# Kernel optimization log

Hardware: AMD Instinct MI355X
Metric: run time of the kernel (lower is better)

Reference implementation:

```python
import jax, jax.numpy as jnp
import numpy as np

D_MODEL = 512
N_HEADS = 8
HEAD_DIM = D_MODEL // N_HEADS
SCALE = float(np.sqrt(HEAD_DIM))


def setup_inputs() -> dict:
    key = jax.random.key(0)
    k1, k2, k3, k4, k5, k6 = jax.random.split(key, 6)
    B, T, S = 4, 2048, 4096
    query = jax.random.normal(k1, (B, T, D_MODEL), dtype=jnp.float32)
    keys = jax.random.normal(k2, (B, S, D_MODEL), dtype=jnp.float32)
    key_padding_mask = jnp.zeros((B, S), dtype=bool)  # all valid
    # Linear params (torch nn.Linear: y = x @ W.T + b)
    lim = 1.0 / np.sqrt(D_MODEL)
    q_w = jax.random.uniform(k3, (D_MODEL, D_MODEL), jnp.float32, -lim, lim)
    q_b = jax.random.uniform(k4, (D_MODEL,), jnp.float32, -lim, lim)
    k_w = jax.random.uniform(k5, (D_MODEL, D_MODEL), jnp.float32, -lim, lim)
    k_b = jax.random.uniform(k6, (D_MODEL,), jnp.float32, -lim, lim)
    return {"query": query, "keys": keys, "key_padding_mask": key_padding_mask,
            "q_w": q_w, "q_b": q_b, "k_w": k_w, "k_b": k_b}


def reference(query, keys, key_padding_mask, q_w, q_b, k_w, k_b):
    B, T, _ = query.shape
    S = keys.shape[1]
    q = (query @ q_w.T + q_b).reshape(B, T, N_HEADS, HEAD_DIM)
    k = (keys @ k_w.T + k_b).reshape(B, S, N_HEADS, HEAD_DIM)
    # mean over heads of scaled per-head QK^T == single contraction over (h,d)
    # divided by n_heads*scale; avoids materializing [B,H,T,S].
    logits = jnp.einsum('bthd,bshd->bts', q, k) / (N_HEADS * SCALE)
    logits = jnp.where(key_padding_mask[:, None, :], -jnp.inf, logits)
    return logits
```

## Files before the change

kernel.cpp:

```cpp
#include <hip/hip_runtime.h>
#include <hip/hip_bf16.h>

using bf16 = __hip_bfloat16;
typedef __attribute__((ext_vector_type(8))) short short8;
typedef __attribute__((ext_vector_type(4))) float floatx4;
typedef __attribute__((ext_vector_type(16))) float floatx16;

#define NEG_INF (-__builtin_huge_valf())

__device__ __forceinline__ void gld_lds16(const void* g, void* l) {
  __builtin_amdgcn_global_load_lds(
      (const __attribute__((address_space(1))) unsigned int*)g,
      (__attribute__((address_space(3))) unsigned int*)l, 16, 0, 0);
}

template <int N> __device__ __forceinline__ void wait_vm() {
  asm volatile("s_waitcnt vmcnt(%0)" ::"n"(N) : "memory");
}
__device__ __forceinline__ void bar() {
  asm volatile("" ::: "memory");
  __builtin_amdgcn_s_barrier();
  asm volatile("" ::: "memory");
}

__device__ __forceinline__ void cvt8(const float4& a, const float4& b, bf16* t) {
  t[0] = __float2bfloat16(a.x); t[1] = __float2bfloat16(a.y);
  t[2] = __float2bfloat16(a.z); t[3] = __float2bfloat16(a.w);
  t[4] = __float2bfloat16(b.x); t[5] = __float2bfloat16(b.y);
  t[6] = __float2bfloat16(b.z); t[7] = __float2bfloat16(b.w);
}

__global__ __launch_bounds__(256) void cvt_in(const float* __restrict__ q,
                                              const float* __restrict__ k,
                                              const float* __restrict__ qw,
                                              const float* __restrict__ kw,
                                              bf16* __restrict__ qo, bf16* __restrict__ ko,
                                              bf16* __restrict__ qwo, bf16* __restrict__ kwo) {
  const size_t e = ((size_t)blockIdx.x * 256 + threadIdx.x) * 8;
  const float* src; bf16* dst;
  if (e < 4194304)       { src = q  + e;              dst = qo  + e; }
  else if (e < 12582912) { src = k  + (e - 4194304);  dst = ko  + (e - 4194304); }
  else if (e < 12845056) { src = qw + (e - 12582912); dst = qwo + (e - 12582912); }
  else                   { src = kw + (e - 12845056); dst = kwo + (e - 12845056); }
  float4 a = *(const float4*)src;
  float4 c = *(const float4*)(src + 4);
  bf16 t[8];
  cvt8(a, c, t);
  *(short8*)dst = *(short8*)t;
}

__device__ __forceinline__ void mfma_tile32(const bf16* sAh, const bf16* sBh,
                                            int wm, int wn, int lane,
                                            floatx16 acc[2][2]) {
  const int fm = lane & 31;
  const int fk = (lane >> 5) * 8;
  #pragma unroll
  for (int ks = 0; ks < 2; ++ks) {
    short8 a0 = *(const short8*)(sAh + (wm +  0 + fm) * 32 + ks * 16 + fk);
    short8 a1 = *(const short8*)(sAh + (wm + 32 + fm) * 32 + ks * 16 + fk);
    short8 b0 = *(const short8*)(sBh + (wn +  0 + fm) * 32 + ks * 16 + fk);
    short8 b1 = *(const short8*)(sBh + (wn + 32 + fm) * 32 + ks * 16 + fk);
    acc[0][0] = __builtin_amdgcn_mfma_f32_32x32x16_bf16(a0, b0, acc[0][0], 0, 0, 0);
    acc[0][1] = __builtin_amdgcn_mfma_f32_32x32x16_bf16(a0, b1, acc[0][1], 0, 0, 0);
    acc[1][0] = __builtin_amdgcn_mfma_f32_32x32x16_bf16(a1, b0, acc[1][0], 0, 0, 0);
    acc[1][1] = __builtin_amdgcn_mfma_f32_32x32x16_bf16(a1, b1, acc[1][1], 0, 0, 0);
  }
}

__global__ __launch_bounds__(256) void proj(const bf16* __restrict__ Xq,
                                            const bf16* __restrict__ Xk,
                                            const bf16* __restrict__ qw,
                                            const bf16* __restrict__ kw,
                                            const float* __restrict__ qb,
                                            const float* __restrict__ kb,
                                            bf16* __restrict__ qo,
                                            bf16* __restrict__ ko) {
  __shared__ bf16 sA[2][128 * 32];
  __shared__ bf16 sB[2][128 * 32];
  const int mt = blockIdx.x;
  const bool isQ = mt < 64;
  const bf16* A    = isQ ? Xq : Xk;
  const bf16* W    = isQ ? qw : kw;
  const float* bias = isQ ? qb : kb;
  bf16* outp       = isQ ? qo : ko;
  const int m0 = (isQ ? mt : mt - 64) * 128;
  const int n0 = blockIdx.y * 128;

  const int tid  = threadIdx.x;
  const int lane = tid & 63;
  const int w    = tid >> 6;
  const int wm   = (w >> 1) * 64;
  const int wn   = (w & 1) * 64;
  const int st_row = lane >> 2;
  const int st_col = (lane & 3) * 8;

  floatx16 acc[2][2];
  #pragma unroll
  for (int mi = 0; mi < 2; ++mi)
    #pragma unroll
    for (int ni = 0; ni < 2; ++ni)
      #pragma unroll
      for (int r = 0; r < 16; ++r)
        acc[mi][ni][r] = 0.f;

  for (int kt = 0; kt < 512; kt += 64) {
    #pragma unroll
    for (int h = 0; h < 2; ++h)
      #pragma unroll
      for (int j = 0; j < 2; ++j) {
        const int r = (w << 5) + (j << 4);
        gld_lds16(A + (size_t)(m0 + r + st_row) * 512 + kt + h * 32 + st_col,
                  &sA[h][r * 32]);
        gld_lds16(W + (size_t)(n0 + r + st_row) * 512 + kt + h * 32 + st_col,
                  &sB[h][r * 32]);
      }
    __syncthreads();
    #pragma unroll
    for (int h = 0; h < 2; ++h)
      mfma_tile32(sA[h], sB[h], wm, wn, lane, acc);
    __syncthreads();
  }

  const int col = lane & 31;
  const int rhi = (lane >> 5) * 4;
  #pragma unroll
  for (int ni = 0; ni < 2; ++ni) {
    const int gn = n0 + wn + ni * 32 + col;
    const float bv = bias[gn];
    #pragma unroll
    for (int mi = 0; mi < 2; ++mi)
      #pragma unroll
      for (int reg = 0; reg < 16; ++reg) {
        const int row = (reg & 3) + 8 * (reg >> 2) + rhi;
        outp[(size_t)(m0 + wm + mi * 32 + row) * 512 + gn] =
            __float2bfloat16(acc[mi][ni][reg] + bv);
      }
  }
}

__global__ __launch_bounds__(512, 2) void qk8(const bf16* __restrict__ Q,
                                              const bf16* __restrict__ Kp,
                                              const unsigned char* __restrict__ mask,
                                              float* __restrict__ out) {
  __shared__ alignas(16) char smem[2][4][16384];

  const int bid = blockIdx.x;
  const int sb  = ((bid & 7) << 6) | (bid >> 3);
  const int b   = sb >> 7;
  const int mt  = (sb >> 4) & 7;
  const int nt  = sb & 15;

  const bf16* Qb = Q  + ((size_t)b * 2048 + (size_t)mt * 256) * 512;
  const bf16* Kb = Kp + ((size_t)b * 4096 + (size_t)nt * 256) * 512;

  const int tid  = threadIdx.x;
  const int lane = tid & 63;
  const int w    = tid >> 6;
  const int wm   = w >> 2;
  const int wn   = w & 3;
  const int l15  = lane & 15;
  const int kg   = lane >> 4;
  const int aoff = l15 * 64 + ((kg << 4) ^ ((l15 & 8) << 2) ^ ((l15 & 2) << 3));

  auto stage = [&](int t) {
    const int kt = t * 64;
    char* dst = &smem[t & 1][0][0];
    #pragma unroll
    for (int hf = 0; hf < 4; ++hf) {
      const bf16* src = (hf < 2) ? Qb : Kb;
      const int rb = (hf & 1) * 128;
      #pragma unroll
      for (int L = 0; L < 2; ++L) {
        const int lin = tid * 16 + L * 8192;
        const int sub = lin >> 10;
        const int r   = ((sub >> 1) << 4) | ((lin >> 6) & 15);
        const int swz = ((r & 8) << 2) ^ ((r & 2) << 3);
        const int cby = ((sub & 1) << 6) | ((lin & 63) ^ swz);
        gld_lds16(src + (size_t)(rb + r) * 512 + kt + (cby >> 1),
                  dst + hf * 16384 + L * 8192 + w * 1024);
      }
    }
  };

  floatx4 acc[8][4];
  #pragma unroll
  for (int i = 0; i < 8; ++i)
    #pragma unroll
    for (int j = 0; j < 4; ++j)
      acc[i][j] = (floatx4){0.f, 0.f, 0.f, 0.f};

  stage(0);
  stage(1);
  wait_vm<8>();
  bar();

  #pragma unroll
  for (int t = 0; t < 8; ++t) {
    const char* Ah = &smem[t & 1][wm][0];
    const char* Bh = &smem[t & 1][2 + (wn >> 1)][0];
    const int bfb = (wn & 1) * 4;
    #pragma unroll
    for (int rh = 0; rh < 2; ++rh) {
      short8 a[4][2];
      #pragma unroll
      for (int fr = 0; fr < 4; ++fr)
        #pragma unroll
        for (int ks = 0; ks < 2; ++ks)
          a[fr][ks] = *(const short8*)(Ah + (rh * 4 + fr) * 2048 + ks * 1024 + aoff);
      #pragma unroll
      for (int ch = 0; ch < 2; ++ch) {
        short8 bb[2][2];
        #pragma unroll
        for (int fn = 0; fn < 2; ++fn)
          #pragma unroll
          for (int ks = 0; ks < 2; ++ks)
            bb[fn][ks] = *(const short8*)(Bh + (bfb + ch * 2 + fn) * 2048 + ks * 1024 + aoff);
        __builtin_amdgcn_s_setprio(1);
        #pragma unroll
        for (int fr = 0; fr < 4; ++fr)
          #pragma unroll
          for (int fn = 0; fn < 2; ++fn)
            #pragma unroll
            for (int ks = 0; ks < 2; ++ks)
              acc[rh * 4 + fr][ch * 2 + fn] = __builtin_amdgcn_mfma_f32_16x16x32_bf16(
                  a[fr][ks], bb[fn][ks], acc[rh * 4 + fr][ch * 2 + fn], 0, 0, 0);
        __builtin_amdgcn_s_setprio(0);
      }
    }
    if (t < 7) {
      bar();
      if (t < 6) { stage(t + 2); wait_vm<8>(); }
      else       { wait_vm<0>(); }
      bar();
    }
  }

  float* ob = out + (size_t)b * 2048 * 4096
                  + ((size_t)mt * 256 + (size_t)wm * 128) * 4096
                  + (size_t)nt * 256 + wn * 64;
  const unsigned char* mb = mask + (size_t)b * 4096 + nt * 256 + wn * 64;
  #pragma unroll
  for (int fc = 0; fc < 4; ++fc) {
    const int c = fc * 16 + l15;
    const bool msk = mb[c] != 0;
    #pragma unroll
    for (int f8 = 0; f8 < 8; ++f8)
      #pragma unroll
      for (int r = 0; r < 4; ++r)
        ob[(size_t)(f8 * 16 + kg * 4 + r) * 4096 + c] =
            msk ? NEG_INF : acc[f8][fc][r] * (1.f / 64.f);
  }
}

extern "C" void kernel_launch(void* const* d_in, const int* in_sizes, int n_in,
                              void* d_out, int out_size, void* d_ws, size_t ws_size,
                              hipStream_t stream) {
  const float* query = (const float*)d_in[0];
  const float* keys  = (const float*)d_in[1];
  const unsigned char* mask = (const unsigned char*)d_in[2];
  const float* q_w = (const float*)d_in[3];
  const float* q_b = (const float*)d_in[4];
  const float* k_w = (const float*)d_in[5];
  const float* k_b = (const float*)d_in[6];
  float* out = (float*)d_out;

  const size_t nq = 4194304;
  const size_t nk = 8388608;
  const size_t nw = 262144;

  char* ws = (char*)d_ws;
  bf16* q_bf   = (bf16*)ws;
  bf16* k_bf   = (bf16*)(ws + nq * 2);
  bf16* qw_bf  = (bf16*)(ws + (nq + nk) * 2);
  bf16* kw_bf  = (bf16*)(ws + (nq + nk + nw) * 2);
  bf16* q_proj = (bf16*)(ws + (nq + nk + 2 * nw) * 2);
  bf16* k_proj = (bf16*)(ws + (2 * nq + nk + 2 * nw) * 2);

  cvt_in<<<6400, 256, 0, stream>>>(query, keys, q_w, k_w, q_bf, k_bf, qw_bf, kw_bf);
  proj<<<dim3(192, 4), 256, 0, stream>>>(q_bf, k_bf, qw_bf, kw_bf, q_b, k_b,
                                         q_proj, k_proj);
  qk8<<<512, 512, 0, stream>>>(q_proj, k_proj, mask, out);
}
```

Baseline: 252.9 us.

## Split K-tile staging into halves and interleave loads with MFMA phases

Global-to-LDS staging is split into per-k-half chunks issued at a finer grain inside the compute loop, so that the next tile's halves load while the current one is computed. The inner loop is restructured into k-half phases with explicit barriers, lgkmcnt waits and sched_barriers, in a ping-pong style that separates LDS reads from MFMA bursts. The intent is smoother overlap of memory and compute and less stall at tile boundaries. The cost is many more barriers per iteration and tighter ordering between the partial stages in the two buffers.

```diff
diff --git a/kernel.cpp b/kernel.cpp
--- a/kernel.cpp
+++ b/kernel.cpp
@@ -162,24 +162,17 @@
   const int kg   = lane >> 4;
   const int aoff = l15 * 64 + ((kg << 4) ^ ((l15 & 8) << 2) ^ ((l15 & 2) << 3));
 
-  auto stage = [&](int t) {
-    const int kt = t * 64;
-    char* dst = &smem[t & 1][0][0];
-    #pragma unroll
-    for (int hf = 0; hf < 4; ++hf) {
-      const bf16* src = (hf < 2) ? Qb : Kb;
-      const int rb = (hf & 1) * 128;
-      #pragma unroll
-      for (int L = 0; L < 2; ++L) {
-        const int lin = tid * 16 + L * 8192;
-        const int sub = lin >> 10;
-        const int r   = ((sub >> 1) << 4) | ((lin >> 6) & 15);
-        const int swz = ((r & 8) << 2) ^ ((r & 2) << 3);
-        const int cby = ((sub & 1) << 6) | ((lin & 63) ^ swz);
-        gld_lds16(src + (size_t)(rb + r) * 512 + kt + (cby >> 1),
-                  dst + hf * 16384 + L * 8192 + w * 1024);
-      }
-    }
+  auto stage_kh = [&](int t, int kh) {
+    const int kt  = t * 64;
+    char* dst = &smem[t & 1][0][0] + (w * 2 + kh) * 1024;
+    const int r   = (w << 4) | (lane >> 2);
+    const int swz = ((r & 8) << 2) ^ ((r & 2) << 3);
+    const int cby = (kh << 6) | ((((lane & 3) << 4)) ^ swz);
+    const int gc  = kt + (cby >> 1);
+    gld_lds16(Qb + (size_t)(      r) * 512 + gc, dst);
+    gld_lds16(Qb + (size_t)(128 + r) * 512 + gc, dst + 16384);
+    gld_lds16(Kb + (size_t)(      r) * 512 + gc, dst + 32768);
+    gld_lds16(Kb + (size_t)(128 + r) * 512 + gc, dst + 49152);
   };
 
   floatx4 acc[8][4];
@@ -189,48 +182,55 @@
     for (int j = 0; j < 4; ++j)
       acc[i][j] = (floatx4){0.f, 0.f, 0.f, 0.f};
 
-  stage(0);
-  stage(1);
-  wait_vm<8>();
+  stage_kh(0, 0); stage_kh(0, 1); stage_kh(1, 0);
+  wait_vm<4>();
   bar();
 
   #pragma unroll
   for (int t = 0; t < 8; ++t) {
     const char* Ah = &smem[t & 1][wm][0];
-    const char* Bh = &smem[t & 1][2 + (wn >> 1)][0];
-    const int bfb = (wn & 1) * 4;
-    #pragma unroll
-    for (int rh = 0; rh < 2; ++rh) {
-      short8 a[4][2];
+    const char* Bh = &smem[t & 1][2 + (wn >> 1)][0] + (wn & 1) * 8192;
+    #pragma unroll
+    for (int kh = 0; kh < 2; ++kh) {
+      short8 a[4], bb[4];
+      if (kh == 0) { if (t < 7) stage_kh(t + 1, 1); }
+      else         { if (t < 6) stage_kh(t + 2, 0); }
+      #pragma unroll
+      for (int fr = 0; fr < 4; ++fr)
+        a[fr] = *(const short8*)(Ah + fr * 2048 + kh * 1024 + aoff);
+      #pragma unroll
+      for (int fn = 0; fn < 4; ++fn)
+        bb[fn] = *(const short8*)(Bh + fn * 2048 + kh * 1024 + aoff);
+      bar();
+      asm volatile("s_waitcnt lgkmcnt(0)" ::: "memory");
+      __builtin_amdgcn_sched_barrier(0);
+      __builtin_amdgcn_s_setprio(1);
       #pragma unroll
       for (int fr = 0; fr < 4; ++fr)
         #pragma unroll
-        for (int ks = 0; ks < 2; ++ks)
-          a[fr][ks] = *(const short8*)(Ah + (rh * 4 + fr) * 2048 + ks * 1024 + aoff);
-      #pragma unroll
-      for (int ch = 0; ch < 2; ++ch) {
-        short8 bb[2][2];
+        for (int fn = 0; fn < 4; ++fn)
+          acc[fr][fn] = __builtin_amdgcn_mfma_f32_16x16x32_bf16(
+              a[fr], bb[fn], acc[fr][fn], 0, 0, 0);
+      __builtin_amdgcn_s_setprio(0);
+      bar();
+      #pragma unroll
+      for (int fr = 0; fr < 4; ++fr)
+        a[fr] = *(const short8*)(Ah + (4 + fr) * 2048 + kh * 1024 + aoff);
+      bar();
+      asm volatile("s_waitcnt lgkmcnt(0)" ::: "memory");
+      __builtin_amdgcn_sched_barrier(0);
+      __builtin_amdgcn_s_setprio(1);
+      #pragma unroll
+      for (int fr = 0; fr < 4; ++fr)
         #pragma unroll
-        for (int fn = 0; fn < 2; ++fn)
-          #pragma unroll
-          for (int ks = 0; ks < 2; ++ks)
-            bb[fn][ks] = *(const short8*)(Bh + (bfb + ch * 2 + fn) * 2048 + ks * 1024 + aoff);
-        __builtin_amdgcn_s_setprio(1);
-        #pragma unroll
-        for (int fr = 0; fr < 4; ++fr)
-          #pragma unroll
-          for (int fn = 0; fn < 2; ++fn)
-            #pragma unroll
-            for (int ks = 0; ks < 2; ++ks)
-              acc[rh * 4 + fr][ch * 2 + fn] = __builtin_amdgcn_mfma_f32_16x16x32_bf16(
-                  a[fr][ks], bb[fn][ks], acc[rh * 4 + fr][ch * 2 + fn], 0, 0, 0);
-        __builtin_amdgcn_s_setprio(0);
+        for (int fn = 0; fn < 4; ++fn)
+          acc[4 + fr][fn] = __builtin_amdgcn_mfma_f32_16x16x32_bf16(
+              a[fr], bb[fn], acc[4 + fr][fn], 0, 0, 0);
+      __builtin_amdgcn_s_setprio(0);
+      if (kh == 1) {
+        if (t < 6)       wait_vm<4>();
+        else if (t == 6) wait_vm<0>();
       }
-    }
-    if (t < 7) {
-      bar();
-      if (t < 6) { stage(t + 2); wait_vm<8>(); }
-      else       { wait_vm<0>(); }
       bar();
     }
   }
```

Result: slower. 261.3 us (+3.3%).
